# Optimization experiments

Hardware: AMD Instinct MI355X
Metric: run time of the kernel (lower is better)

## Reference

```python
import jax, jax.numpy as jnp
import numpy as np

UNITS = 32
WIDTH = 64
EPS = 1e-7  # keras.backend.epsilon()


def setup_inputs() -> dict:
    key = jax.random.key(0)
    ks = jax.random.split(key, 6)
    B, L, D = 4, 1024, 128
    x = jax.random.normal(ks[0], (B, L, D), dtype=jnp.float32)
    # glorot-normal-ish scaled params
    Wt = jax.random.normal(ks[1], (D, UNITS), dtype=jnp.float32) * (1.0 / np.sqrt(D))
    Wx = jax.random.normal(ks[2], (D, UNITS), dtype=jnp.float32) * (1.0 / np.sqrt(D))
    bh = jnp.zeros((UNITS,), dtype=jnp.float32)
    Wa = jax.random.normal(ks[3], (UNITS, 1), dtype=jnp.float32) * (1.0 / np.sqrt(UNITS))
    ba = jnp.zeros((1,), dtype=jnp.float32)
    return {"x": x, "Wt": Wt, "Wx": Wx, "bh": bh, "Wa": Wa, "ba": ba}


def reference(x, Wt, Wx, bh, Wa, ba):
    # Additive (Bahdanau-style) self-attention emission.
    B, L, D = x.shape
    q = jnp.einsum('bld,du->blu', x, Wt)  # [B,L,U]
    k = jnp.einsum('bld,du->blu', x, Wx)  # [B,L,U]
    # h: [B, Lq, Lk, U] -- dominant intermediate
    h = jnp.tanh(q[:, :, None, :] + k[:, None, :, :] + bh)
    e = jnp.einsum('bqku,u->bqk', h, Wa[:, 0]) + ba[0]  # [B,L,L]
    # stable exp (unnormalized softmax numerator)
    e = jnp.exp(e - jnp.max(e, axis=-1, keepdims=True))
    # local window mask: lower = i - width//2 ; keep lower <= j < lower + width
    idx = jnp.arange(L)
    lower = idx[:, None] - WIDTH // 2
    win = ((lower <= idx[None, :]) & (idx[None, :] < lower + WIDTH)).astype(e.dtype)
    e = e * win
    a = e / (jnp.sum(e, axis=-1, keepdims=True) + EPS)  # [B,L,L]
    v = jnp.einsum('bqk,bkd->bqd', a, x)  # [B,L,D]
    return v
```

## Files before the change

kernel.cpp:

```cpp
#include <hip/hip_runtime.h>
#include <math.h>

#define BB 4
#define LL 1024
#define DD 128
#define UU 32
#define WW 64
#define HALF 32

__global__ __launch_bounds__(256) void qk_kernel(
    const float* __restrict__ x, const float* __restrict__ Wt,
    const float* __restrict__ Wx, const float* __restrict__ bh,
    float* __restrict__ q, float* __restrict__ kT)
{
    __shared__ float xs[4][DD];
    const int tid = threadIdx.x;
    const int w = tid >> 6, lane = tid & 63;
    const int row = blockIdx.x * 4 + w;
    const float* xr = x + (size_t)row * DD;
    if (lane < 32) ((float4*)xs[w])[lane] = ((const float4*)xr)[lane];
    __syncthreads();
    const int u = lane & 31;
    const bool isQ = (lane < 32);
    const float* Wm = isQ ? Wt : Wx;
    float acc = 0.f;
    #pragma unroll 8
    for (int d = 0; d < DD; ++d)
        acc = fmaf(xs[w][d], Wm[d * UU + u], acc);
    if (isQ) {
        q[(size_t)row * UU + u] = acc + bh[u];
    } else {
        const int b = row >> 10, l = row & (LL - 1);
        kT[((size_t)(b * UU + u)) * LL + l] = acc;
    }
}

#define RPB 8
#define XR  71
#define XRP 72

__global__ __launch_bounds__(256) void attn_kernel(
    const float* __restrict__ x, const float* __restrict__ q,
    const float* __restrict__ kT, const float* __restrict__ Wa,
    float* __restrict__ out)
{
    __shared__ float xs[XRP][DD];
    __shared__ float kts[UU][XRP];
    __shared__ float qs[RPB][UU];
    __shared__ float was[UU];
    __shared__ float as[4][2][WW];

    const int tid = threadIdx.x;
    const int blk = blockIdx.x;
    const int b  = blk >> 7;
    const int i0 = (blk & 127) * RPB;
    const int j0 = i0 - HALF;

    const float* xb = x + (size_t)b * LL * DD;

    {
        const float4* xb4 = (const float4*)xb;
        for (int s = tid; s < XRP * (DD / 4); s += 256) {
            const int r = s >> 5;
            const int c = s & 31;
            int jg = j0 + r; jg = min(max(jg, 0), LL - 1);
            ((float4*)xs)[s] = xb4[jg * (DD / 4) + c];
        }
    }
    {
        const float* kb = kT + (size_t)b * UU * LL;
        for (int s = tid; s < UU * XRP; s += 256) {
            const int u = s / XRP;
            const int r = s - u * XRP;
            int jg = j0 + r; jg = min(max(jg, 0), LL - 1);
            kts[u][r] = kb[(size_t)u * LL + jg];
        }
    }
    ((float*)qs)[tid] = q[((size_t)(b * LL + i0)) * UU + tid];
    if (tid < UU) was[tid] = Wa[tid];
    __syncthreads();

    const int w = tid >> 6, lane = tid & 63;

    #pragma unroll
    for (int rr = 0; rr < 2; ++rr) {
        const int ir = w * 2 + rr;
        const int i  = i0 + ir;
        const int j  = i - HALF + lane;
        const bool valid = (j >= 0) && (j < LL);

        float acc = 0.f;
        #pragma unroll
        for (int u = 0; u < UU; ++u) {
            const float t = qs[ir][u] + kts[u][ir + lane];
            const float ex = __expf(2.f * t);
            acc = fmaf(was[u], fmaf(-2.f, __builtin_amdgcn_rcpf(ex + 1.f), 1.f), acc);
        }
        const float e = valid ? acc : -INFINITY;

        float m = e;
        #pragma unroll
        for (int off = 32; off > 0; off >>= 1)
            m = fmaxf(m, __shfl_xor(m, off));
        const float p = valid ? __expf(e - m) : 0.f;
        float s = p;
        #pragma unroll
        for (int off = 32; off > 0; off >>= 1)
            s += __shfl_xor(s, off);
        const float a = p * __builtin_amdgcn_rcpf(s + 1e-7f);
        as[w][rr][lane] = a;

        float v0 = 0.f, v1 = 0.f;
        #pragma unroll 8
        for (int l = 0; l < WW; ++l) {
            const float al = as[w][rr][l];
            const float2 xv = ((const float2*)xs[ir + l])[lane];
            v0 = fmaf(al, xv.x, v0);
            v1 = fmaf(al, xv.y, v1);
        }
        float2 o; o.x = v0; o.y = v1;
        ((float2*)(out + ((size_t)(b * LL + i)) * DD))[lane] = o;
    }
}

extern "C" void kernel_launch(void* const* d_in, const int* in_sizes, int n_in,
                              void* d_out, int out_size, void* d_ws, size_t ws_size,
                              hipStream_t stream) {
    const float* x  = (const float*)d_in[0];
    const float* Wt = (const float*)d_in[1];
    const float* Wx = (const float*)d_in[2];
    const float* bh = (const float*)d_in[3];
    const float* Wa = (const float*)d_in[4];
    float* out = (float*)d_out;

    float* q  = (float*)d_ws;
    float* kT = q + (size_t)BB * LL * UU;

    qk_kernel<<<BB * LL / 4, 256, 0, stream>>>(x, Wt, Wx, bh, q, kT);
    attn_kernel<<<BB * (LL / RPB), 256, 0, stream>>>(x, q, kT, Wa, out);
}
```

Before: 83.16 us.

## Fuse Q/K projection into attention kernel, recomputing K per window tile

Merges the separate projection kernel into the attention kernel. Each block now computes K for its 72-row window from the x tile already in shared memory, using Wx staged in LDS, and computes Q for its 8 rows. This removes one launch and the global round trip for q and kT. In exchange each K row is recomputed about 9 times across overlapping windows, and LDS use grows by 16KB for Wx, which may reduce occupancy.

```diff
diff --git a/kernel.cpp b/kernel.cpp
--- a/kernel.cpp
+++ b/kernel.cpp
@@ -7,81 +7,87 @@
 #define UU 32
 #define WW 64
 #define HALF 32
+#define RPB 8
+#define XR  72
 
-__global__ __launch_bounds__(256) void qk_kernel(
+__global__ __launch_bounds__(256) void fused_attn(
     const float* __restrict__ x, const float* __restrict__ Wt,
     const float* __restrict__ Wx, const float* __restrict__ bh,
-    float* __restrict__ q, float* __restrict__ kT)
+    const float* __restrict__ Wa, float* __restrict__ out)
 {
-    __shared__ float xs[4][DD];
-    const int tid = threadIdx.x;
-    const int w = tid >> 6, lane = tid & 63;
-    const int row = blockIdx.x * 4 + w;
-    const float* xr = x + (size_t)row * DD;
-    if (lane < 32) ((float4*)xs[w])[lane] = ((const float4*)xr)[lane];
-    __syncthreads();
-    const int u = lane & 31;
-    const bool isQ = (lane < 32);
-    const float* Wm = isQ ? Wt : Wx;
-    float acc = 0.f;
-    #pragma unroll 8
-    for (int d = 0; d < DD; ++d)
-        acc = fmaf(xs[w][d], Wm[d * UU + u], acc);
-    if (isQ) {
-        q[(size_t)row * UU + u] = acc + bh[u];
-    } else {
-        const int b = row >> 10, l = row & (LL - 1);
-        kT[((size_t)(b * UU + u)) * LL + l] = acc;
-    }
-}
-
-#define RPB 8
-#define XR  71
-#define XRP 72
-
-__global__ __launch_bounds__(256) void attn_kernel(
-    const float* __restrict__ x, const float* __restrict__ q,
-    const float* __restrict__ kT, const float* __restrict__ Wa,
-    float* __restrict__ out)
-{
-    __shared__ float xs[XRP][DD];
-    __shared__ float kts[UU][XRP];
+    __shared__ float xs[XR][DD];
+    __shared__ float wxs[DD][UU];
+    __shared__ float kts[UU][XR];
     __shared__ float qs[RPB][UU];
     __shared__ float was[UU];
     __shared__ float as[4][2][WW];
 
     const int tid = threadIdx.x;
     const int blk = blockIdx.x;
-    const int b  = blk >> 7;
-    const int i0 = (blk & 127) * RPB;
-    const int j0 = i0 - HALF;
+    const int b   = blk >> 7;
+    const int i0  = (blk & 127) * RPB;
+    const int j0  = i0 - HALF;
 
     const float* xb = x + (size_t)b * LL * DD;
 
     {
         const float4* xb4 = (const float4*)xb;
-        for (int s = tid; s < XRP * (DD / 4); s += 256) {
-            const int r = s >> 5;
-            const int c = s & 31;
+        float4* xs4 = (float4*)xs;
+        #pragma unroll
+        for (int t = 0; t < 9; ++t) {
+            const int s = tid + t * 256;
+            const int r = s >> 5, c = s & 31;
             int jg = j0 + r; jg = min(max(jg, 0), LL - 1);
-            ((float4*)xs)[s] = xb4[jg * (DD / 4) + c];
+            xs4[s] = xb4[jg * (DD / 4) + c];
         }
     }
     {
-        const float* kb = kT + (size_t)b * UU * LL;
-        for (int s = tid; s < UU * XRP; s += 256) {
-            const int u = s / XRP;
-            const int r = s - u * XRP;
-            int jg = j0 + r; jg = min(max(jg, 0), LL - 1);
-            kts[u][r] = kb[(size_t)u * LL + jg];
-        }
+        const float4* w4 = (const float4*)Wx;
+        float4* wx4 = (float4*)wxs;
+        #pragma unroll
+        for (int t = 0; t < 4; ++t)
+            wx4[tid + t * 256] = w4[tid + t * 256];
     }
-    ((float*)qs)[tid] = q[((size_t)(b * LL + i0)) * UU + tid];
     if (tid < UU) was[tid] = Wa[tid];
     __syncthreads();
 
+    const int r0 = tid >> 5, u = tid & 31;
+
+    {
+        float acc[9];
+        #pragma unroll
+        for (int k = 0; k < 9; ++k) acc[k] = 0.f;
+        #pragma unroll 4
+        for (int d4 = 0; d4 < DD / 4; ++d4) {
+            const float w0 = wxs[4 * d4 + 0][u];
+            const float w1 = wxs[4 * d4 + 1][u];
+            const float w2 = wxs[4 * d4 + 2][u];
+            const float w3 = wxs[4 * d4 + 3][u];
+            #pragma unroll
+            for (int k = 0; k < 9; ++k) {
+                const float4 xv = ((const float4*)xs[r0 + 8 * k])[d4];
+                acc[k] = fmaf(xv.x, w0, fmaf(xv.y, w1,
+                         fmaf(xv.z, w2, fmaf(xv.w, w3, acc[k]))));
+            }
+        }
+        #pragma unroll
+        for (int k = 0; k < 9; ++k) kts[u][r0 + 8 * k] = acc[k];
+    }
+    {
+        float acc = bh[u];
+        #pragma unroll 4
+        for (int d4 = 0; d4 < DD / 4; ++d4) {
+            const float4 xv = ((const float4*)xs[HALF + r0])[d4];
+            acc = fmaf(xv.x, Wt[(4 * d4 + 0) * UU + u],
+                  fmaf(xv.y, Wt[(4 * d4 + 1) * UU + u],
+                  fmaf(xv.z, Wt[(4 * d4 + 2) * UU + u],
+                  fmaf(xv.w, Wt[(4 * d4 + 3) * UU + u], acc))));
+        }
+        qs[r0][u] = acc;
+    }
+    __syncthreads();
+
     const int w = tid >> 6, lane = tid & 63;
-
     #pragma unroll
     for (int rr = 0; rr < 2; ++rr) {
         const int ir = w * 2 + rr;
@@ -91,10 +97,10 @@
 
         float acc = 0.f;
         #pragma unroll
-        for (int u = 0; u < UU; ++u) {
-            const float t = qs[ir][u] + kts[u][ir + lane];
+        for (int uu = 0; uu < UU; ++uu) {
+            const float t = qs[ir][uu] + kts[uu][ir + lane];
             const float ex = __expf(2.f * t);
-            acc = fmaf(was[u], fmaf(-2.f, __builtin_amdgcn_rcpf(ex + 1.f), 1.f), acc);
+            acc = fmaf(was[uu], fmaf(-2.f, __builtin_amdgcn_rcpf(ex + 1.f), 1.f), acc);
         }
         const float e = valid ? acc : -INFINITY;
 
@@ -133,9 +139,5 @@
     const float* Wa = (const float*)d_in[4];
     float* out = (float*)d_out;
 
-    float* q  = (float*)d_ws;
-    float* kT = q + (size_t)BB * LL * UU;
-
-    qk_kernel<<<BB * LL / 4, 256, 0, stream>>>(x, Wt, Wx, bh, q, kT);
-    attn_kernel<<<BB * (LL / RPB), 256, 0, stream>>>(x, q, kT, Wa, out);
+    fused_attn<<<BB * (LL / RPB), 256, 0, stream>>>(x, Wt, Wx, bh, Wa, out);
 }
```

New measurement: 81.18 us. 2.4% less time.
